# Kernel tuning notes

Measured on AMD Instinct MI355X. Metric: run time of the kernel, lower is better.

Reference implementation:

```python
import jax, jax.numpy as jnp
import numpy as np
import math

B, S, D, H, L, F = 32, 512, 512, 8, 4, 1024
TD = 4 * D  # time embedding dim
DH = D // H
SCALE = 1.0 / math.sqrt(DH)


def _ln(x, g, b):
    m = jnp.mean(x, -1, keepdims=True)
    v = jnp.var(x, -1, keepdims=True)
    return (x - m) * jax.lax.rsqrt(v + 1e-5) * g + b


def setup_inputs() -> dict:
    key = jax.random.key(0)
    ks = jax.random.split(key, 12)
    w = lambda k, shp: jax.random.normal(k, shp, dtype=jnp.float32) * 0.02
    return {
        "x": jax.random.normal(ks[0], (B, S, D), dtype=jnp.float32),
        "time": jax.random.uniform(ks[1], (B,), dtype=jnp.float32) * 1000.0,
        "time_w1": w(ks[2], (TD, D)), "time_b1": jnp.zeros((TD,), jnp.float32),
        "time_w2": w(ks[3], (TD, TD)), "time_b2": jnp.zeros((TD,), jnp.float32),
        "Wq": w(ks[4], (L, D, D)), "bq": jnp.zeros((L, D), jnp.float32),
        "Wk": w(ks[5], (L, D, D)), "bk": jnp.zeros((L, D), jnp.float32),
        "Wv": w(ks[6], (L, D, D)), "bv": jnp.zeros((L, D), jnp.float32),
        "Wo": w(ks[7], (L, D, D)), "bo": jnp.zeros((L, D), jnp.float32),
        "attn_g": jnp.ones((L, D), jnp.float32), "attn_b": jnp.zeros((L, D), jnp.float32),
        "ffn_g": jnp.ones((L, D), jnp.float32), "ffn_b": jnp.zeros((L, D), jnp.float32),
        "W1": w(ks[8], (L, 2 * F, D)), "b1": jnp.zeros((L, 2 * F), jnp.float32),
        "W2": w(ks[9], (L, D, F)), "b2": jnp.zeros((L, D), jnp.float32),
        "Wt": w(ks[10], (L, 4 * F, TD)), "bt": jnp.zeros((L, 4 * F), jnp.float32),
        "head_g": jnp.ones((D,), jnp.float32), "head_b": jnp.zeros((D,), jnp.float32),
        "Wh": w(ks[11], (D, D)), "bh": jnp.zeros((D,), jnp.float32),
    }


def _forward(x, time, time_w1, time_b1, time_w2, time_b2,
             Wq, bq, Wk, bk, Wv, bv, Wo, bo,
             attn_g, attn_b, ffn_g, ffn_b,
             W1, b1, W2, b2, Wt, bt,
             head_g, head_b, Wh, bh):
    Bsz = x.shape[0]
    # --- sinusoidal time embedding + time MLP ---
    half = D // 2
    freqs = jnp.exp(jnp.arange(half, dtype=jnp.float32) * (-math.log(10000.0) / (half - 1)))
    e = time[:, None] * freqs[None, :]
    temb = jnp.concatenate([jnp.sin(e), jnp.cos(e)], axis=-1)  # [B, D]
    temb = jax.nn.gelu(temb @ time_w1.T + time_b1, approximate=False) @ time_w2.T + time_b2  # [B, 4D]
    for i in range(L):
        # attention (prenorm; block 0 skips the norm since first_prenormalization=False)
        h = x if i == 0 else _ln(x, attn_g[i], attn_b[i])
        q = (h @ Wq[i].T + bq[i]).reshape(Bsz, S, H, DH)
        k = (h @ Wk[i].T + bk[i]).reshape(Bsz, S, H, DH)
        v = (h @ Wv[i].T + bv[i]).reshape(Bsz, S, H, DH)
        logits = jnp.einsum('bqhd,bkhd->bhqk', q, k) * SCALE
        probs = jax.nn.softmax(logits, axis=-1)
        o = jnp.einsum('bhqk,bkhd->bqhd', probs, v).reshape(Bsz, S, D)
        x = x + (o @ Wo[i].T + bo[i])
        # FFN with FiLM time conditioning and ReGLU activation
        h = _ln(x, ffn_g[i], ffn_b[i])
        h1 = h @ W1[i].T + b1[i]  # [B, S, 2F]
        tm = jax.nn.silu(temb) @ Wt[i].T + bt[i]  # [B, 4F]
        scale, shift = jnp.split(tm[:, None, :], 2, axis=-1)  # each [B, 1, 2F]
        h1 = h1 * (scale + 1.0) + shift
        a, g = jnp.split(h1, 2, axis=-1)  # ReGLU: a * relu(g)
        x = x + ((a * jax.nn.relu(g)) @ W2[i].T + b2[i])
    # head: last token -> LayerNorm -> ReLU -> Linear
    z = _ln(x[:, -1], head_g, head_b)
    return jax.nn.relu(z) @ Wh.T + bh


def reference(x, time, time_w1, time_b1, time_w2, time_b2,
              Wq, bq, Wk, bk, Wv, bv, Wo, bo,
              attn_g, attn_b, ffn_g, ffn_b,
              W1, b1, W2, b2, Wt, bt,
              head_g, head_b, Wh, bh):
    return _forward(x, time, time_w1, time_b1, time_w2, time_b2,
                    Wq, bq, Wk, bk, Wv, bv, Wo, bo,
                    attn_g, attn_b, ffn_g, ffn_b,
                    W1, b1, W2, b2, Wt, bt,
                    head_g, head_b, Wh, bh)
```

## Files before the change

kernel.cpp:

```cpp
#include <hip/hip_runtime.h>
#include <math.h>

typedef __bf16 bf16_t;
typedef __bf16 bf16x8 __attribute__((ext_vector_type(8)));
typedef float f32x4 __attribute__((ext_vector_type(4)));

__device__ __forceinline__ void gload_lds16(const void* g, void* l) {
    __builtin_amdgcn_global_load_lds(
        (const __attribute__((address_space(1))) void*)g,
        (__attribute__((address_space(3))) void*)l, 16, 0, 0);
}

__global__ void k_f2b(const float* __restrict__ in, bf16_t* __restrict__ out, int n8) {
    int idx = blockIdx.x * 256 + threadIdx.x;
    if (idx >= n8) return;
    const float* p = in + (size_t)idx * 8;
    bf16x8 r;
#pragma unroll
    for (int j = 0; j < 8; j++) r[j] = (bf16_t)p[j];
    *(bf16x8*)(out + (size_t)idx * 8) = r;
}

__global__ void k_time_embed(const float* __restrict__ time, float* __restrict__ temb0) {
    int b = blockIdx.x;
    int j = threadIdx.x;
    float f = __expf((float)j * -0.036118981458730134f);
    float e = time[b] * f;
    temb0[(size_t)b * 512 + j] = sinf(e);
    temb0[(size_t)b * 512 + 256 + j] = cosf(e);
}

template<bool DO_NORM>
__global__ void k_ln(const float* __restrict__ x, const float* __restrict__ g,
                     const float* __restrict__ b, bf16_t* __restrict__ out) {
    int row = blockIdx.x * 4 + (threadIdx.x >> 6);
    int lane = threadIdx.x & 63;
    const float* xr = x + (size_t)row * 512 + lane * 8;
    float4 v0 = *(const float4*)xr;
    float4 v1 = *(const float4*)(xr + 4);
    float vals[8] = {v0.x, v0.y, v0.z, v0.w, v1.x, v1.y, v1.z, v1.w};
    bf16x8 r;
    if (DO_NORM) {
        float s = 0.f, sq = 0.f;
#pragma unroll
        for (int j = 0; j < 8; j++) { s += vals[j]; sq += vals[j] * vals[j]; }
#pragma unroll
        for (int m = 1; m < 64; m <<= 1) { s += __shfl_xor(s, m, 64); sq += __shfl_xor(sq, m, 64); }
        float mean = s * (1.0f / 512.0f);
        float var = sq * (1.0f / 512.0f) - mean * mean;
        float rstd = rsqrtf(var + 1e-5f);
        float4 g0 = *(const float4*)(g + lane * 8);
        float4 g1 = *(const float4*)(g + lane * 8 + 4);
        float4 b0 = *(const float4*)(b + lane * 8);
        float4 b1 = *(const float4*)(b + lane * 8 + 4);
        float gs[8] = {g0.x, g0.y, g0.z, g0.w, g1.x, g1.y, g1.z, g1.w};
        float bs[8] = {b0.x, b0.y, b0.z, b0.w, b1.x, b1.y, b1.z, b1.w};
#pragma unroll
        for (int j = 0; j < 8; j++) r[j] = (bf16_t)((vals[j] - mean) * rstd * gs[j] + bs[j]);
    } else {
#pragma unroll
        for (int j = 0; j < 8; j++) r[j] = (bf16_t)vals[j];
    }
    *(bf16x8*)(out + (size_t)row * 512 + lane * 8) = r;
}

__global__ void k_head_prep(const float* __restrict__ x, const float* __restrict__ g,
                            const float* __restrict__ b, float* __restrict__ z) {
    int row = blockIdx.x * 4 + (threadIdx.x >> 6);
    int lane = threadIdx.x & 63;
    const float* xr = x + ((size_t)row * 512 + 511) * 512 + lane * 8;
    float4 v0 = *(const float4*)xr;
    float4 v1 = *(const float4*)(xr + 4);
    float vals[8] = {v0.x, v0.y, v0.z, v0.w, v1.x, v1.y, v1.z, v1.w};
    float s = 0.f, sq = 0.f;
#pragma unroll
    for (int j = 0; j < 8; j++) { s += vals[j]; sq += vals[j] * vals[j]; }
#pragma unroll
    for (int m = 1; m < 64; m <<= 1) { s += __shfl_xor(s, m, 64); sq += __shfl_xor(sq, m, 64); }
    float mean = s * (1.0f / 512.0f);
    float var = sq * (1.0f / 512.0f) - mean * mean;
    float rstd = rsqrtf(var + 1e-5f);
    float o[8];
#pragma unroll
    for (int j = 0; j < 8; j++) {
        float gv = g[lane * 8 + j], bv = b[lane * 8 + j];
        o[j] = fmaxf((vals[j] - mean) * rstd * gv + bv, 0.0f);
    }
    float* zr = z + (size_t)row * 512 + lane * 8;
    *(float4*)zr = make_float4(o[0], o[1], o[2], o[3]);
    *(float4*)(zr + 4) = make_float4(o[4], o[5], o[6], o[7]);
}

template<int ACT, int K>
__global__ __launch_bounds__(256, 2)
void k_gemm_tm(const float* __restrict__ A, const float* __restrict__ W,
               const float* __restrict__ bias, float* __restrict__ out, int N) {
    __shared__ float Asm[32][516];
    const int t = threadIdx.x;
    const int kq = t & 7, rw = (t >> 3) & 7, bh = t >> 6;
    const int n0 = blockIdx.x * 32;
    float acc[4][8] = {};
    for (int k0 = 0; k0 < K; k0 += 512) {
        __syncthreads();
#pragma unroll
        for (int i = 0; i < 16; i++) {
            int fid = t + i * 256;
            int row = fid >> 7, cc = (fid & 127) << 2;
            *(float4*)&Asm[row][cc] = *(const float4*)&A[(size_t)row * K + k0 + cc];
        }
        __syncthreads();
#pragma unroll 4
        for (int j = 0; j < 16; j++) {
            int kk = kq * 4 + j * 32;
            float4 w4[4];
#pragma unroll
            for (int r = 0; r < 4; r++)
                w4[r] = *(const float4*)&W[(size_t)(n0 + rw + r * 8) * K + k0 + kk];
#pragma unroll
            for (int b = 0; b < 8; b++) {
                float4 a4 = *(const float4*)&Asm[bh * 8 + b][kk];
#pragma unroll
                for (int r = 0; r < 4; r++)
                    acc[r][b] += a4.x * w4[r].x + a4.y * w4[r].y + a4.z * w4[r].z + a4.w * w4[r].w;
            }
        }
    }
#pragma unroll
    for (int m = 1; m < 8; m <<= 1)
#pragma unroll
        for (int r = 0; r < 4; r++)
#pragma unroll
            for (int b = 0; b < 8; b++)
                acc[r][b] += __shfl_xor(acc[r][b], m, 64);
    if (kq == 0) {
#pragma unroll
        for (int r = 0; r < 4; r++) {
            int n = n0 + rw + r * 8;
            float bv = bias[n];
#pragma unroll
            for (int b = 0; b < 8; b++) {
                float v = acc[r][b] + bv;
                if (ACT == 1) v = 0.5f * v * (1.0f + erff(v * 0.70710678118654752f));
                if (ACT == 2) v = v / (1.0f + __expf(-v));
                out[(size_t)(bh * 8 + b) * N + n] = v;
            }
        }
    }
}

enum { EPI_QKV = 0, EPI_RESID = 1, EPI_FILMGLU = 2 };

template<int EPI, int K>
__global__ __launch_bounds__(256, 4)
void k_gemm_bt(const bf16_t* __restrict__ A, const bf16_t* __restrict__ W,
               const float* __restrict__ bias, const float* __restrict__ bias2,
               const float* __restrict__ bias3,
               void* __restrict__ out0, void* __restrict__ out1, void* __restrict__ out2,
               const float* __restrict__ tm) {
    __shared__ __align__(16) bf16_t Abuf[128 * 64];
    __shared__ __align__(16) bf16_t Bbuf[128 * 64];
    const int tid = threadIdx.x;
    const int bx = blockIdx.x, by = blockIdx.y;
    const int m0 = bx * 128;
    const int lane = tid & 63;
    const int wave = tid >> 6;
    const int wr = (wave >> 1) * 64, wc = (wave & 1) * 64;

    const int srow = tid >> 3;
    const int goff = ((tid & 7) * 16) ^ ((srow & 7) << 4);
    const char* Ag = (const char*)A;
    const char* Wg = (const char*)W;
    char* AbL = (char*)Abuf + tid * 16;
    char* BbL = (char*)Bbuf + tid * 16;
    int growB[4];
#pragma unroll
    for (int i = 0; i < 4; i++) {
        int r = srow + i * 32;
        if (EPI == EPI_FILMGLU) {
            int half = (r >> 5) & 1;
            int base = by * 64 + (r >> 6) * 32 + (r & 31);
            growB[i] = half * 1024 + base;
        } else {
            growB[i] = by * 128 + r;
        }
    }

    f32x4 acc[4][4] = {};
    for (int k0 = 0; k0 < K * 2; k0 += 128) {
        __syncthreads();
#pragma unroll
        for (int i = 0; i < 4; i++) {
            gload_lds16(Ag + (size_t)(m0 + srow + i * 32) * (K * 2) + k0 + goff, AbL + i * 4096);
            gload_lds16(Wg + (size_t)growB[i] * (K * 2) + k0 + goff, BbL + i * 4096);
        }
        __syncthreads();
#pragma unroll
        for (int kk = 0; kk < 2; kk++) {
            bf16x8 af[4], bfr[4];
#pragma unroll
            for (int i = 0; i < 4; i++) {
                int ar = wr + i * 16 + (lane & 15);
                af[i] = *(const bf16x8*)((const char*)Abuf + ar * 128 +
                         ((kk * 64 + (lane >> 4) * 16) ^ ((ar & 7) << 4)));
                int br = wc + i * 16 + (lane & 15);
                bfr[i] = *(const bf16x8*)((const char*)Bbuf + br * 128 +
                         ((kk * 64 + (lane >> 4) * 16) ^ ((br & 7) << 4)));
            }
#pragma unroll
            for (int i = 0; i < 4; i++)
#pragma unroll
                for (int j = 0; j < 4; j++)
                    acc[i][j] = __builtin_amdgcn_mfma_f32_16x16x32_bf16(af[i], bfr[j], acc[i][j], 0, 0, 0);
        }
    }

    const int b = m0 >> 9;
    if (EPI == EPI_QKV) {
        const int which = by >> 2;
        bf16_t* op = (bf16_t*)(which == 0 ? out0 : which == 1 ? out1 : out2);
        const float* bp = which == 0 ? bias : which == 1 ? bias2 : bias3;
#pragma unroll
        for (int i = 0; i < 4; i++) {
#pragma unroll
            for (int r = 0; r < 4; r++) {
                int s = (m0 + wr + i * 16 + (lane >> 4) * 4 + r) & 511;
#pragma unroll
                for (int j = 0; j < 4; j++) {
                    int c = (by & 3) * 128 + wc + j * 16 + (lane & 15);
                    float v = acc[i][j][r] + bp[c];
                    int h = c >> 6, dh = c & 63;
                    op[(((size_t)b * 8 + h) * 512 + s) * 64 + dh] = (bf16_t)v;
                }
            }
        }
    } else if (EPI == EPI_RESID) {
        float* op = (float*)out0;
        const float* rs = (const float*)out1;
#pragma unroll
        for (int i = 0; i < 4; i++) {
#pragma unroll
            for (int r = 0; r < 4; r++) {
                int row = m0 + wr + i * 16 + (lane >> 4) * 4 + r;
#pragma unroll
                for (int j = 0; j < 4; j++) {
                    int col = by * 128 + wc + j * 16 + (lane & 15);
                    size_t idx = (size_t)row * 512 + col;
                    op[idx] = rs[idx] + acc[i][j][r] + bias[col];
                }
            }
        }
    } else {
        bf16_t* op = (bf16_t*)out0;
        const float* tml = tm + (size_t)b * 16384;
#pragma unroll
        for (int i = 0; i < 4; i++) {
#pragma unroll
            for (int r = 0; r < 4; r++) {
                int row = m0 + wr + i * 16 + (lane >> 4) * 4 + r;
#pragma unroll
                for (int jj = 0; jj < 2; jj++) {
                    int colA = by * 64 + (wave & 1) * 32 + jj * 16 + (lane & 15);
                    float av = acc[i][jj][r] + bias[colA];
                    float gv = acc[i][jj + 2][r] + bias[1024 + colA];
                    av = av * (1.0f + tml[colA]) + tml[2048 + colA];
                    gv = gv * (1.0f + tml[1024 + colA]) + tml[3072 + colA];
                    op[(size_t)row * 1024 + colA] = (bf16_t)(av * fmaxf(gv, 0.0f));
                }
            }
        }
    }
}

__global__ __launch_bounds__(256, 2)
void k_attn(const bf16_t* __restrict__ q, const bf16_t* __restrict__ k,
            const bf16_t* __restrict__ v, bf16_t* __restrict__ o) {
    __shared__ bf16_t q_lds[64][72];
    __shared__ bf16_t k_lds[64][72];
    __shared__ bf16_t vt_lds[64][72];
    __shared__ bf16_t p_lds[64][72];
    const int tid = threadIdx.x;
    const int lane = tid & 63;
    const int wave = tid >> 6;
    const int qt = blockIdx.x;
    const int bh = blockIdx.y;
    const bf16_t* qb = q + ((size_t)bh * 512 + qt * 64) * 64;
    const bf16_t* kb = k + (size_t)bh * 512 * 64;
    const bf16_t* vb = v + (size_t)bh * 512 * 64;
    const int sr = tid >> 2;
    const int sc = (tid & 3) * 16;
    {
        bf16x8 a0 = *(const bf16x8*)(qb + sr * 64 + sc);
        bf16x8 a1 = *(const bf16x8*)(qb + sr * 64 + sc + 8);
        bf16x8 ra, rb;
#pragma unroll
        for (int j = 0; j < 8; j++) {
            ra[j] = (bf16_t)((float)a0[j] * 0.125f);
            rb[j] = (bf16_t)((float)a1[j] * 0.125f);
        }
        *(bf16x8*)&q_lds[sr][sc] = ra;
        *(bf16x8*)&q_lds[sr][sc + 8] = rb;
    }
    float mrow[4], lrow[4];
    f32x4 oacc[4] = {};
#pragma unroll
    for (int r = 0; r < 4; r++) { mrow[r] = -1e30f; lrow[r] = 0.f; }
    for (int kt = 0; kt < 8; kt++) {
        __syncthreads();
        {
            const bf16_t* ks = kb + ((size_t)kt * 64 + sr) * 64 + sc;
            const bf16_t* vs = vb + ((size_t)kt * 64 + sr) * 64 + sc;
            *(bf16x8*)&k_lds[sr][sc] = *(const bf16x8*)ks;
            *(bf16x8*)&k_lds[sr][sc + 8] = *(const bf16x8*)(ks + 8);
            bf16x8 v0 = *(const bf16x8*)vs;
            bf16x8 v1 = *(const bf16x8*)(vs + 8);
#pragma unroll
            for (int j = 0; j < 8; j++) {
                vt_lds[sc + j][sr] = v0[j];
                vt_lds[sc + 8 + j][sr] = v1[j];
            }
        }
        __syncthreads();
        f32x4 sacc[4] = {};
#pragma unroll
        for (int kk = 0; kk < 2; kk++) {
            bf16x8 aq = *(const bf16x8*)&q_lds[wave * 16 + (lane & 15)][kk * 32 + (lane >> 4) * 8];
#pragma unroll
            for (int c = 0; c < 4; c++) {
                bf16x8 bk8 = *(const bf16x8*)&k_lds[c * 16 + (lane & 15)][kk * 32 + (lane >> 4) * 8];
                sacc[c] = __builtin_amdgcn_mfma_f32_16x16x32_bf16(aq, bk8, sacc[c], 0, 0, 0);
            }
        }
#pragma unroll
        for (int r = 0; r < 4; r++) {
            float mx = fmaxf(fmaxf(sacc[0][r], sacc[1][r]), fmaxf(sacc[2][r], sacc[3][r]));
#pragma unroll
            for (int m = 1; m < 16; m <<= 1) mx = fmaxf(mx, __shfl_xor(mx, m, 64));
            float newm = fmaxf(mrow[r], mx);
            float fsc = __expf(mrow[r] - newm);
            mrow[r] = newm;
            float p0 = __expf(sacc[0][r] - newm);
            float p1 = __expf(sacc[1][r] - newm);
            float p2 = __expf(sacc[2][r] - newm);
            float p3 = __expf(sacc[3][r] - newm);
            float ps = p0 + p1 + p2 + p3;
#pragma unroll
            for (int m = 1; m < 16; m <<= 1) ps += __shfl_xor(ps, m, 64);
            lrow[r] = lrow[r] * fsc + ps;
#pragma unroll
            for (int c = 0; c < 4; c++) oacc[c][r] *= fsc;
            int qrow = wave * 16 + (lane >> 4) * 4 + r;
            p_lds[qrow][(lane & 15)] = (bf16_t)p0;
            p_lds[qrow][16 + (lane & 15)] = (bf16_t)p1;
            p_lds[qrow][32 + (lane & 15)] = (bf16_t)p2;
            p_lds[qrow][48 + (lane & 15)] = (bf16_t)p3;
        }
        __syncthreads();
#pragma unroll
        for (int kk = 0; kk < 2; kk++) {
            bf16x8 ap = *(const bf16x8*)&p_lds[wave * 16 + (lane & 15)][kk * 32 + (lane >> 4) * 8];
#pragma unroll
            for (int c = 0; c < 4; c++) {
                bf16x8 bv8 = *(const bf16x8*)&vt_lds[c * 16 + (lane & 15)][kk * 32 + (lane >> 4) * 8];
                oacc[c] = __builtin_amdgcn_mfma_f32_16x16x32_bf16(ap, bv8, oacc[c], 0, 0, 0);
            }
        }
    }
    const int b = bh >> 3, h = bh & 7;
#pragma unroll
    for (int r = 0; r < 4; r++) {
        int s = qt * 64 + wave * 16 + (lane >> 4) * 4 + r;
        float inv = 1.0f / lrow[r];
#pragma unroll
        for (int c = 0; c < 4; c++) {
            o[((size_t)b * 512 + s) * 512 + h * 64 + c * 16 + (lane & 15)] = (bf16_t)(oacc[c][r] * inv);
        }
    }
}

extern "C" void kernel_launch(void* const* d_in, const int* in_sizes, int n_in,
                              void* d_out, int out_size, void* d_ws, size_t ws_size,
                              hipStream_t stream) {
    const float* x_in   = (const float*)d_in[0];
    const float* time_in= (const float*)d_in[1];
    const float* tw1    = (const float*)d_in[2];
    const float* tb1    = (const float*)d_in[3];
    const float* tw2    = (const float*)d_in[4];
    const float* tb2    = (const float*)d_in[5];
    const float* Wq     = (const float*)d_in[6];
    const float* bq     = (const float*)d_in[7];
    const float* Wk     = (const float*)d_in[8];
    const float* bk     = (const float*)d_in[9];
    const float* Wv     = (const float*)d_in[10];
    const float* bv     = (const float*)d_in[11];
    const float* Wo     = (const float*)d_in[12];
    const float* bo     = (const float*)d_in[13];
    const float* attn_g = (const float*)d_in[14];
    const float* attn_b = (const float*)d_in[15];
    const float* ffn_g  = (const float*)d_in[16];
    const float* ffn_b  = (const float*)d_in[17];
    const float* W1     = (const float*)d_in[18];
    const float* b1     = (const float*)d_in[19];
    const float* W2     = (const float*)d_in[20];
    const float* b2     = (const float*)d_in[21];
    const float* Wt     = (const float*)d_in[22];
    const float* bt     = (const float*)d_in[23];
    const float* head_g = (const float*)d_in[24];
    const float* head_b = (const float*)d_in[25];
    const float* Wh     = (const float*)d_in[26];
    const float* bh     = (const float*)d_in[27];

    size_t off = 0;
    auto alloc = [&](size_t bytes) {
        void* r = (char*)d_ws + off;
        off += (bytes + 255) & ~(size_t)255;
        return r;
    };
    bf16_t* wqkv_b = (bf16_t*)alloc((size_t)4 * 3 * 512 * 512 * 2);
    bf16_t* wo_b   = (bf16_t*)alloc((size_t)4 * 512 * 512 * 2);
    bf16_t* w1_b   = (bf16_t*)alloc((size_t)4 * 2048 * 512 * 2);
    bf16_t* w2_b   = (bf16_t*)alloc((size_t)4 * 512 * 1024 * 2);
    float*  x_ws   = (float*)alloc((size_t)16384 * 512 * 4);
    bf16_t* h_b    = (bf16_t*)alloc((size_t)16384 * 512 * 2);
    bf16_t* q_b    = (bf16_t*)alloc((size_t)16384 * 512 * 2);
    bf16_t* k_b    = (bf16_t*)alloc((size_t)16384 * 512 * 2);
    bf16_t* v_b    = (bf16_t*)alloc((size_t)16384 * 512 * 2);
    bf16_t* o_b    = (bf16_t*)alloc((size_t)16384 * 512 * 2);
    bf16_t* act_b  = (bf16_t*)alloc((size_t)16384 * 1024 * 2);
    float*  temb0  = (float*)alloc((size_t)32 * 512 * 4);
    float*  t1     = (float*)alloc((size_t)32 * 2048 * 4);
    float*  t2s    = (float*)alloc((size_t)32 * 2048 * 4);
    float*  tm_all = (float*)alloc((size_t)32 * 16384 * 4);
    float*  z      = (float*)alloc((size_t)32 * 512 * 4);

    for (int l = 0; l < 4; l++) {
        k_f2b<<<128, 256, 0, stream>>>(Wq + (size_t)l * 262144, wqkv_b + ((size_t)l * 3 + 0) * 262144, 32768);
        k_f2b<<<128, 256, 0, stream>>>(Wk + (size_t)l * 262144, wqkv_b + ((size_t)l * 3 + 1) * 262144, 32768);
        k_f2b<<<128, 256, 0, stream>>>(Wv + (size_t)l * 262144, wqkv_b + ((size_t)l * 3 + 2) * 262144, 32768);
    }
    k_f2b<<<512, 256, 0, stream>>>(Wo, wo_b, 131072);
    k_f2b<<<2048, 256, 0, stream>>>(W1, w1_b, 524288);
    k_f2b<<<1024, 256, 0, stream>>>(W2, w2_b, 262144);

    k_time_embed<<<32, 256, 0, stream>>>(time_in, temb0);
    k_gemm_tm<1, 512><<<64, 256, 0, stream>>>(temb0, tw1, tb1, t1, 2048);
    k_gemm_tm<2, 2048><<<64, 256, 0, stream>>>(t1, tw2, tb2, t2s, 2048);
    k_gemm_tm<0, 2048><<<512, 256, 0, stream>>>(t2s, Wt, bt, tm_all, 16384);

    for (int l = 0; l < 4; l++) {
        if (l == 0)
            k_ln<false><<<4096, 256, 0, stream>>>(x_in, nullptr, nullptr, h_b);
        else
            k_ln<true><<<4096, 256, 0, stream>>>(x_ws, attn_g + l * 512, attn_b + l * 512, h_b);

        k_gemm_bt<EPI_QKV, 512><<<dim3(128, 12), 256, 0, stream>>>(
            h_b, wqkv_b + (size_t)l * 786432,
            bq + l * 512, bk + l * 512, bv + l * 512,
            q_b, k_b, v_b, nullptr);

        k_attn<<<dim3(8, 256), 256, 0, stream>>>(q_b, k_b, v_b, o_b);

        k_gemm_bt<EPI_RESID, 512><<<dim3(128, 4), 256, 0, stream>>>(
            o_b, wo_b + (size_t)l * 262144,
            bo + l * 512, nullptr, nullptr,
            x_ws, (void*)(l == 0 ? x_in : x_ws), nullptr, nullptr);

        k_ln<true><<<4096, 256, 0, stream>>>(x_ws, ffn_g + l * 512, ffn_b + l * 512, h_b);

        k_gemm_bt<EPI_FILMGLU, 512><<<dim3(128, 16), 256, 0, stream>>>(
            h_b, w1_b + (size_t)l * 1048576,
            b1 + l * 2048, nullptr, nullptr,
            act_b, nullptr, nullptr, tm_all + l * 4096);

        k_gemm_bt<EPI_RESID, 1024><<<dim3(128, 4), 256, 0, stream>>>(
            act_b, w2_b + (size_t)l * 524288,
            b2 + l * 512, nullptr, nullptr,
            x_ws, x_ws, nullptr, nullptr);
    }

    k_head_prep<<<8, 256, 0, stream>>>(x_ws, head_g, head_b, z);
    k_gemm_tm<0, 512><<<16, 256, 0, stream>>>(z, Wh, bh, (float*)d_out, 512);
}
```

Measured before the change: 1.178 ms.

## Use MFMA split-K for time-modulation GEMM, remap workgroups, prefetch K/V in attention

Several independent changes land together. The large time-conditioning projection (Wt times the time MLP output) moves from an FP32 FMA kernel to a bf16 MFMA split-K kernel that writes a transposed result with atomicAdd after a bias prefill, and the FiLM epilogue reads that transposed layout. The bt GEMMs use a 1D grid with XCD-aware block remapping to improve L2 locality across the chiplets, QKV weight conversion collapses into three strided launches, and attention register-prefetches the next K/V tile while using a swizzled V-transpose LDS layout to cut bank conflicts. The attention change also drops the barrier between writing and reading p_lds; that is likely still safe only because each wave reads back just its own rows. The bf16 conversion of Wt and of the time MLP output, plus the atomic accumulation, adds rounding and nondeterminism.

```diff
diff --git a/kernel.cpp b/kernel.cpp
--- a/kernel.cpp
+++ b/kernel.cpp
@@ -19,6 +19,17 @@
 #pragma unroll
     for (int j = 0; j < 8; j++) r[j] = (bf16_t)p[j];
     *(bf16x8*)(out + (size_t)idx * 8) = r;
+}
+
+__global__ void k_f2b_s(const float* __restrict__ in, bf16_t* __restrict__ out,
+                        int seg8, int dstride8) {
+    int idx = blockIdx.x * 256 + threadIdx.x;
+    int seg = idx / seg8, rem = idx - seg * seg8;
+    const float* p = in + (size_t)idx * 8;
+    bf16x8 r;
+#pragma unroll
+    for (int j = 0; j < 8; j++) r[j] = (bf16_t)p[j];
+    *(bf16x8*)(out + ((size_t)seg * dstride8 + rem) * 8) = r;
 }
 
 __global__ void k_time_embed(const float* __restrict__ time, float* __restrict__ temb0) {
@@ -91,10 +102,10 @@
     *(float4*)(zr + 4) = make_float4(o[4], o[5], o[6], o[7]);
 }
 
-template<int ACT, int K>
+template<int ACT, int K, bool OUTB>
 __global__ __launch_bounds__(256, 2)
 void k_gemm_tm(const float* __restrict__ A, const float* __restrict__ W,
-               const float* __restrict__ bias, float* __restrict__ out, int N) {
+               const float* __restrict__ bias, void* __restrict__ outp, int N) {
     __shared__ float Asm[32][516];
     const int t = threadIdx.x;
     const int kq = t & 7, rw = (t >> 3) & 7, bh = t >> 6;
@@ -142,15 +153,80 @@
                 float v = acc[r][b] + bv;
                 if (ACT == 1) v = 0.5f * v * (1.0f + erff(v * 0.70710678118654752f));
                 if (ACT == 2) v = v / (1.0f + __expf(-v));
-                out[(size_t)(bh * 8 + b) * N + n] = v;
-            }
-        }
-    }
+                if (OUTB) ((bf16_t*)outp)[(size_t)(bh * 8 + b) * N + n] = (bf16_t)v;
+                else      ((float*)outp)[(size_t)(bh * 8 + b) * N + n] = v;
+            }
+        }
+    }
+}
+
+__global__ void k_fill_tmt(const float* __restrict__ bt, float* __restrict__ tm_t) {
+    int i = blockIdx.x * 256 + threadIdx.x;
+    tm_t[i] = bt[i >> 5];
+}
+
+__global__ __launch_bounds__(256, 4)
+void k_gemm_wt(const float* __restrict__ Wt, const bf16_t* __restrict__ t2s_b,
+               float* __restrict__ tm_t) {
+    __shared__ __align__(16) bf16_t Abuf[64 * 64];
+    __shared__ __align__(16) bf16_t Bbuf[32 * 64];
+    const int tid = threadIdx.x;
+    const int m0 = blockIdx.x * 64;
+    const int k0 = blockIdx.y * 512;
+    const int lane = tid & 63, wave = tid >> 6;
+    const int arow = tid >> 2, aseg = tid & 3;
+    const int brow = tid >> 3, bseg = tid & 7;
+    const int aswz = (arow & 7) << 4;
+    const char* Bg = (const char*)t2s_b + (size_t)brow * 4096 + ((bseg * 16) ^ ((brow & 7) << 4));
+    char* BbL = (char*)Bbuf + tid * 16;
+    const float* Ar0 = Wt + (size_t)(m0 + arow) * 2048 + k0 + aseg * 16;
+    f32x4 acc[2] = {};
+    for (int kk0 = 0; kk0 < 512; kk0 += 64) {
+        float4 a4[4];
+#pragma unroll
+        for (int i = 0; i < 4; i++) a4[i] = *(const float4*)(Ar0 + kk0 + i * 4);
+        __syncthreads();
+        gload_lds16(Bg + (size_t)(k0 + kk0) * 2, BbL);
+        bf16x8 c0, c1;
+#pragma unroll
+        for (int i = 0; i < 4; i++) {
+            const float* af = (const float*)&a4[i];
+#pragma unroll
+            for (int j = 0; j < 4; j++) {
+                if (i < 2) c0[i * 4 + j] = (bf16_t)af[j];
+                else       c1[(i - 2) * 4 + j] = (bf16_t)af[j];
+            }
+        }
+        int base = arow * 128 + aseg * 32;
+        *(bf16x8*)((char*)Abuf + (base ^ aswz)) = c0;
+        *(bf16x8*)((char*)Abuf + ((base + 16) ^ aswz)) = c1;
+        __syncthreads();
+#pragma unroll
+        for (int kk = 0; kk < 2; kk++) {
+            int ar = wave * 16 + (lane & 15);
+            bf16x8 af = *(const bf16x8*)((const char*)Abuf + ar * 128 +
+                        ((kk * 64 + (lane >> 4) * 16) ^ ((ar & 7) << 4)));
+#pragma unroll
+            for (int j = 0; j < 2; j++) {
+                int br = j * 16 + (lane & 15);
+                bf16x8 bfr = *(const bf16x8*)((const char*)Bbuf + br * 128 +
+                             ((kk * 64 + (lane >> 4) * 16) ^ ((br & 7) << 4)));
+                acc[j] = __builtin_amdgcn_mfma_f32_16x16x32_bf16(af, bfr, acc[j], 0, 0, 0);
+            }
+        }
+    }
+#pragma unroll
+    for (int j = 0; j < 2; j++)
+#pragma unroll
+        for (int r = 0; r < 4; r++) {
+            int mrow = m0 + wave * 16 + (lane >> 4) * 4 + r;
+            atomicAdd(&tm_t[(size_t)mrow * 32 + j * 16 + (lane & 15)], acc[j][r]);
+        }
 }
 
 enum { EPI_QKV = 0, EPI_RESID = 1, EPI_FILMGLU = 2 };
 
-template<int EPI, int K>
+template<int EPI, int K, int NBY>
 __global__ __launch_bounds__(256, 4)
 void k_gemm_bt(const bf16_t* __restrict__ A, const bf16_t* __restrict__ W,
                const float* __restrict__ bias, const float* __restrict__ bias2,
@@ -160,7 +236,10 @@
     __shared__ __align__(16) bf16_t Abuf[128 * 64];
     __shared__ __align__(16) bf16_t Bbuf[128 * 64];
     const int tid = threadIdx.x;
-    const int bx = blockIdx.x, by = blockIdx.y;
+    const int cpx = gridDim.x >> 3;
+    const int wg = (blockIdx.x & 7) * cpx + (blockIdx.x >> 3);
+    const int bx = wg / NBY;
+    const int by = wg - bx * NBY;
     const int m0 = bx * 128;
     const int lane = tid & 63;
     const int wave = tid >> 6;
@@ -251,7 +330,6 @@
         }
     } else {
         bf16_t* op = (bf16_t*)out0;
-        const float* tml = tm + (size_t)b * 16384;
 #pragma unroll
         for (int i = 0; i < 4; i++) {
 #pragma unroll
@@ -262,8 +340,12 @@
                     int colA = by * 64 + (wave & 1) * 32 + jj * 16 + (lane & 15);
                     float av = acc[i][jj][r] + bias[colA];
                     float gv = acc[i][jj + 2][r] + bias[1024 + colA];
-                    av = av * (1.0f + tml[colA]) + tml[2048 + colA];
-                    gv = gv * (1.0f + tml[1024 + colA]) + tml[3072 + colA];
+                    float sa = tm[(size_t)colA * 32 + b];
+                    float ha = tm[(size_t)(2048 + colA) * 32 + b];
+                    float sg = tm[(size_t)(1024 + colA) * 32 + b];
+                    float hg = tm[(size_t)(3072 + colA) * 32 + b];
+                    av = av * (1.0f + sa) + ha;
+                    gv = gv * (1.0f + sg) + hg;
                     op[(size_t)row * 1024 + colA] = (bf16_t)(av * fmaxf(gv, 0.0f));
                 }
             }
@@ -276,7 +358,7 @@
             const bf16_t* __restrict__ v, bf16_t* __restrict__ o) {
     __shared__ bf16_t q_lds[64][72];
     __shared__ bf16_t k_lds[64][72];
-    __shared__ bf16_t vt_lds[64][72];
+    __shared__ bf16_t vt_lds[64 * 72];
     __shared__ bf16_t p_lds[64][72];
     const int tid = threadIdx.x;
     const int lane = tid & 63;
@@ -300,26 +382,40 @@
         *(bf16x8*)&q_lds[sr][sc] = ra;
         *(bf16x8*)&q_lds[sr][sc + 8] = rb;
     }
+    bf16x8 kr0, kr1, vr0, vr1;
+    {
+        const bf16_t* ks = kb + (size_t)sr * 64 + sc;
+        const bf16_t* vs = vb + (size_t)sr * 64 + sc;
+        kr0 = *(const bf16x8*)ks; kr1 = *(const bf16x8*)(ks + 8);
+        vr0 = *(const bf16x8*)vs; vr1 = *(const bf16x8*)(vs + 8);
+    }
     float mrow[4], lrow[4];
     f32x4 oacc[4] = {};
 #pragma unroll
     for (int r = 0; r < 4; r++) { mrow[r] = -1e30f; lrow[r] = 0.f; }
+    const int swz0 = ((sc >> 3) & 7) << 4;
+    const int swz1 = (((sc + 8) >> 3) & 7) << 4;
     for (int kt = 0; kt < 8; kt++) {
         __syncthreads();
         {
-            const bf16_t* ks = kb + ((size_t)kt * 64 + sr) * 64 + sc;
-            const bf16_t* vs = vb + ((size_t)kt * 64 + sr) * 64 + sc;
-            *(bf16x8*)&k_lds[sr][sc] = *(const bf16x8*)ks;
-            *(bf16x8*)&k_lds[sr][sc + 8] = *(const bf16x8*)(ks + 8);
-            bf16x8 v0 = *(const bf16x8*)vs;
-            bf16x8 v1 = *(const bf16x8*)(vs + 8);
+            *(bf16x8*)&k_lds[sr][sc] = kr0;
+            *(bf16x8*)&k_lds[sr][sc + 8] = kr1;
+            char* vbase = (char*)vt_lds;
+            int so0 = (sr * 2) ^ swz0;
+            int so1 = (sr * 2) ^ swz1;
 #pragma unroll
             for (int j = 0; j < 8; j++) {
-                vt_lds[sc + j][sr] = v0[j];
-                vt_lds[sc + 8 + j][sr] = v1[j];
-            }
-        }
-        __syncthreads();
+                *(bf16_t*)(vbase + (sc + j) * 144 + so0) = vr0[j];
+                *(bf16_t*)(vbase + (sc + 8 + j) * 144 + so1) = vr1[j];
+            }
+        }
+        __syncthreads();
+        if (kt < 7) {
+            const bf16_t* ks = kb + ((size_t)(kt + 1) * 64 + sr) * 64 + sc;
+            const bf16_t* vs = vb + ((size_t)(kt + 1) * 64 + sr) * 64 + sc;
+            kr0 = *(const bf16x8*)ks; kr1 = *(const bf16x8*)(ks + 8);
+            vr0 = *(const bf16x8*)vs; vr1 = *(const bf16x8*)(vs + 8);
+        }
         f32x4 sacc[4] = {};
 #pragma unroll
         for (int kk = 0; kk < 2; kk++) {
@@ -354,13 +450,15 @@
             p_lds[qrow][32 + (lane & 15)] = (bf16_t)p2;
             p_lds[qrow][48 + (lane & 15)] = (bf16_t)p3;
         }
-        __syncthreads();
 #pragma unroll
         for (int kk = 0; kk < 2; kk++) {
             bf16x8 ap = *(const bf16x8*)&p_lds[wave * 16 + (lane & 15)][kk * 32 + (lane >> 4) * 8];
 #pragma unroll
             for (int c = 0; c < 4; c++) {
-                bf16x8 bv8 = *(const bf16x8*)&vt_lds[c * 16 + (lane & 15)][kk * 32 + (lane >> 4) * 8];
+                int d0 = c * 16 + (lane & 15);
+                int xo = ((d0 >> 3) & 7) << 4;
+                bf16x8 bv8 = *(const bf16x8*)((const char*)vt_lds + d0 * 144 +
+                              ((kk * 64 + (lane >> 4) * 16) ^ xo));
                 oacc[c] = __builtin_amdgcn_mfma_f32_16x16x32_bf16(ap, bv8, oacc[c], 0, 0, 0);
             }
         }
@@ -428,23 +526,22 @@
     bf16_t* act_b  = (bf16_t*)alloc((size_t)16384 * 1024 * 2);
     float*  temb0  = (float*)alloc((size_t)32 * 512 * 4);
     float*  t1     = (float*)alloc((size_t)32 * 2048 * 4);
-    float*  t2s    = (float*)alloc((size_t)32 * 2048 * 4);
-    float*  tm_all = (float*)alloc((size_t)32 * 16384 * 4);
+    bf16_t* t2s_b  = (bf16_t*)alloc((size_t)32 * 2048 * 2);
+    float*  tm_t   = (float*)alloc((size_t)16384 * 32 * 4);
     float*  z      = (float*)alloc((size_t)32 * 512 * 4);
 
-    for (int l = 0; l < 4; l++) {
-        k_f2b<<<128, 256, 0, stream>>>(Wq + (size_t)l * 262144, wqkv_b + ((size_t)l * 3 + 0) * 262144, 32768);
-        k_f2b<<<128, 256, 0, stream>>>(Wk + (size_t)l * 262144, wqkv_b + ((size_t)l * 3 + 1) * 262144, 32768);
-        k_f2b<<<128, 256, 0, stream>>>(Wv + (size_t)l * 262144, wqkv_b + ((size_t)l * 3 + 2) * 262144, 32768);
-    }
+    k_f2b_s<<<512, 256, 0, stream>>>(Wq, wqkv_b,          32768, 98304);
+    k_f2b_s<<<512, 256, 0, stream>>>(Wk, wqkv_b + 262144, 32768, 98304);
+    k_f2b_s<<<512, 256, 0, stream>>>(Wv, wqkv_b + 524288, 32768, 98304);
     k_f2b<<<512, 256, 0, stream>>>(Wo, wo_b, 131072);
     k_f2b<<<2048, 256, 0, stream>>>(W1, w1_b, 524288);
     k_f2b<<<1024, 256, 0, stream>>>(W2, w2_b, 262144);
 
     k_time_embed<<<32, 256, 0, stream>>>(time_in, temb0);
-    k_gemm_tm<1, 512><<<64, 256, 0, stream>>>(temb0, tw1, tb1, t1, 2048);
-    k_gemm_tm<2, 2048><<<64, 256, 0, stream>>>(t1, tw2, tb2, t2s, 2048);
-    k_gemm_tm<0, 2048><<<512, 256, 0, stream>>>(t2s, Wt, bt, tm_all, 16384);
+    k_gemm_tm<1, 512, false><<<64, 256, 0, stream>>>(temb0, tw1, tb1, t1, 2048);
+    k_gemm_tm<2, 2048, true><<<64, 256, 0, stream>>>(t1, tw2, tb2, t2s_b, 2048);
+    k_fill_tmt<<<2048, 256, 0, stream>>>(bt, tm_t);
+    k_gemm_wt<<<dim3(256, 4), 256, 0, stream>>>(Wt, t2s_b, tm_t);
 
     for (int l = 0; l < 4; l++) {
         if (l == 0)
@@ -452,31 +549,31 @@
         else
             k_ln<true><<<4096, 256, 0, stream>>>(x_ws, attn_g + l * 512, attn_b + l * 512, h_b);
 
-        k_gemm_bt<EPI_QKV, 512><<<dim3(128, 12), 256, 0, stream>>>(
+        k_gemm_bt<EPI_QKV, 512, 12><<<1536, 256, 0, stream>>>(
             h_b, wqkv_b + (size_t)l * 786432,
             bq + l * 512, bk + l * 512, bv + l * 512,
             q_b, k_b, v_b, nullptr);
 
         k_attn<<<dim3(8, 256), 256, 0, stream>>>(q_b, k_b, v_b, o_b);
 
-        k_gemm_bt<EPI_RESID, 512><<<dim3(128, 4), 256, 0, stream>>>(
+        k_gemm_bt<EPI_RESID, 512, 4><<<512, 256, 0, stream>>>(
             o_b, wo_b + (size_t)l * 262144,
             bo + l * 512, nullptr, nullptr,
             x_ws, (void*)(l == 0 ? x_in : x_ws), nullptr, nullptr);
 
         k_ln<true><<<4096, 256, 0, stream>>>(x_ws, ffn_g + l * 512, ffn_b + l * 512, h_b);
 
-        k_gemm_bt<EPI_FILMGLU, 512><<<dim3(128, 16), 256, 0, stream>>>(
+        k_gemm_bt<EPI_FILMGLU, 512, 16><<<2048, 256, 0, stream>>>(
             h_b, w1_b + (size_t)l * 1048576,
             b1 + l * 2048, nullptr, nullptr,
-            act_b, nullptr, nullptr, tm_all + l * 4096);
-
-        k_gemm_bt<EPI_RESID, 1024><<<dim3(128, 4), 256, 0, stream>>>(
+            act_b, nullptr, nullptr, tm_t + (size_t)l * 4096 * 32);
+
+        k_gemm_bt<EPI_RESID, 1024, 4><<<512, 256, 0, stream>>>(
             act_b, w2_b + (size_t)l * 524288,
             b2 + l * 512, nullptr, nullptr,
             x_ws, x_ws, nullptr, nullptr);
     }
 
     k_head_prep<<<8, 256, 0, stream>>>(x_ws, head_g, head_b, z);
-    k_gemm_tm<0, 512><<<16, 256, 0, stream>>>(z, Wh, bh, (float*)d_out, 512);
-}
+    k_gemm_tm<0, 512, false><<<16, 256, 0, stream>>>(z, Wh, bh, (float*)d_out, 512);
+}
```

Result: faster. 1.155 ms (-2.0%).
